# Kernel tuning notes

Hardware: AMD Instinct MI355X
Metric: run time of the kernel (lower is better)

Reference implementation:

```python
import jax, jax.numpy as jnp
import numpy as np


def setup_inputs() -> dict:
    key = jax.random.key(0)
    k1, k2 = jax.random.split(key)
    B, C, N = 8, 11, 64  # batch, fragment channels, cubic voxel grid edge
    inp = jax.random.normal(k1, (B, C, N, N, N), dtype=jnp.float32)
    tar = jax.random.normal(k2, (B, C, N, N, N), dtype=jnp.float32)
    # 20 contiguous bins spanning [-4, 4]; bin_range[k] = (lo_k, hi_k)
    edges = jnp.linspace(-4.0, 4.0, 21, dtype=jnp.float32)
    bin_range = jnp.stack([edges[:-1], edges[1:]], axis=-1)  # [20, 2]
    return {"inp": inp, "tar": tar, "bin_range": bin_range}


def _bin_data(x, bin_range):
    # x: [B, C, nx, ny, nz] -> normalized histogram [B, C, K]
    B, C = x.shape[0], x.shape[1]
    nvox = x.shape[2] * x.shape[3] * x.shape[4]
    xf = x.reshape(B, C, -1)  # [B, C, nvox]

    def count_one_bin(b):  # b: [2] = (lo, hi)
        return jnp.sum((xf >= b[0]) & (xf < b[1]), axis=-1).astype(jnp.float32)

    # sequential over K bins (small, fixed) to avoid a [K,B,C,nvox] mask blowup
    counts = jax.lax.map(count_one_bin, bin_range)  # [K, B, C]
    return jnp.transpose(counts, (1, 2, 0)) / jnp.float32(nvox)


def _smooth_l1(a, b):
    # torch.nn.SmoothL1Loss default: beta=1.0, mean reduction
    d = jnp.abs(a - b)
    return jnp.mean(jnp.where(d < 1.0, 0.5 * d * d, d - 0.5))


def reference(inp, tar, bin_range):
    loss1 = _smooth_l1(inp, tar)
    loss2 = jnp.mean(jnp.abs(_bin_data(inp, bin_range) - _bin_data(tar, bin_range)))
    return 0.5 * loss1 + 0.5 * loss2
```

## Files before the change

kernel.cpp:

```cpp
#include <hip/hip_runtime.h>

#define BC 88
#define NVOX 262144
#define KBINS 20
#define THREADS 256
#define NBLOCKS 1024
#define CPB 22
#define CPC 256
#define HSTRIDE 23
#define ROWSET (64 * HSTRIDE)

__global__ void __launch_bounds__(THREADS)
binloss_main(const float* __restrict__ inp, const float* __restrict__ tar,
             const float* __restrict__ br, int* __restrict__ slot,
             int* __restrict__ bslot, float* __restrict__ partials)
{
    __shared__ int   rows[2 * ROWSET];
    __shared__ int   qsum[2][4][KBINS];
    __shared__ float wsum[THREADS / 64];

    const int tid  = threadIdx.x;
    const int lane = tid & 63;
    for (int i = tid; i < 2 * ROWSET; i += THREADS) rows[i] = 0;

    const float e0     = br[0];
    const float eK     = br[2 * KBINS - 1];
    const float inv_w  = (float)KBINS / (eK - e0);
    const float shift1 = 1.0f - e0 * inv_w;
    const float tmax   = 21.5f;
    __syncthreads();

    const int fc  = blockIdx.x * CPB;
    const int ch0 = fc >> 8;
    const int rem = fc & (CPC - 1);
    const int n1  = (rem + CPB > CPC) ? (CPC - rem) : CPB;

    const float4* pa = (const float4*)inp + (size_t)fc * 256 + tid;
    const float4* pb = (const float4*)tar + (size_t)fc * 256 + tid;

    int* r0 = &rows[lane * HSTRIDE];
    int* r1 = r0 + ROWSET;

    float s_lin = 0.f, s_quad = 0.f;

#pragma unroll 2
    for (int k = 0; k < CPB; ++k) {
        float4 a = pa[k * 256];
        float4 b = pb[k * 256];
        int* rw = (k < n1) ? r0 : r1;
#pragma unroll
        for (int q = 0; q < 4; ++q) {
            float av = (&a.x)[q], bv = (&b.x)[q];
            float d = fabsf(av - bv);
            s_lin += fmaxf(d, 1.0f);
            float m = fminf(d, 1.0f);
            s_quad  = __builtin_fmaf(m, m, s_quad);
            int sa = (int)__builtin_amdgcn_fmed3f(__builtin_fmaf(av, inv_w, shift1), 0.0f, tmax);
            int sb = (int)__builtin_amdgcn_fmed3f(__builtin_fmaf(bv, inv_w, shift1), 0.0f, tmax);
            atomicAdd(&rw[sa], 1);
            atomicAdd(&rw[sb], -1);
        }
    }

    float sl1 = (s_lin - (float)(CPB * 4)) + 0.5f * s_quad;
#pragma unroll
    for (int off = 32; off > 0; off >>= 1) sl1 += __shfl_down(sl1, off, 64);
    if (lane == 0) wsum[tid >> 6] = sl1;
    __syncthreads();

    if (tid < 160) {
        const int set = tid / 80, r = tid % 80;
        const int qr = r / KBINS, j = r % KBINS;
        int s = 0;
#pragma unroll
        for (int rr = qr * 16; rr < qr * 16 + 16; ++rr)
            s += rows[set * ROWSET + rr * HSTRIDE + 1 + j];
        qsum[set][qr][j] = s;
    }
    if (tid == 0)
        partials[blockIdx.x] = wsum[0] + wsum[1] + wsum[2] + wsum[3];
    __syncthreads();

    if (tid < 2 * KBINS) {
        const int set = tid / KBINS, j = tid % KBINS;
        int v = qsum[set][0][j] + qsum[set][1][j] + qsum[set][2][j] + qsum[set][3][j];
        if (set == 0)          slot[blockIdx.x * KBINS + j] = v;
        else if (n1 < CPB)     bslot[(ch0 + 1) * KBINS + j] = v;
    }
    if (rem == 0 && tid < KBINS) bslot[ch0 * KBINS + tid] = 0;
}

__global__ void __launch_bounds__(256)
binloss_final(const int* __restrict__ slot, const int* __restrict__ bslot,
              const float* __restrict__ partials, float* __restrict__ out)
{
    __shared__ double r1[256];
    __shared__ double r2[256];
    const int tid = threadIdx.x;
    double s1 = 0.0, s2 = 0.0;
    for (int i = tid; i < NBLOCKS; i += 256) s1 += (double)partials[i];
    for (int i = tid; i < BC * KBINS; i += 256) {
        const int c = i / KBINS, j = i - c * KBINS;
        const int b0 = (128 * c + 10) / 11;
        const int b1 = (128 * (c + 1) + 10) / 11;
        int s = bslot[c * KBINS + j];
        for (int b = b0; b < b1; ++b) s += slot[b * KBINS + j];
        s2 += fabs((double)s);
    }
    r1[tid] = s1; r2[tid] = s2;
    __syncthreads();
    for (int off = 128; off > 0; off >>= 1) {
        if (tid < off) { r1[tid] += r1[tid + off]; r2[tid] += r2[tid + off]; }
        __syncthreads();
    }
    if (tid == 0) {
        const double ntot  = (double)BC * (double)NVOX;
        double loss1 = r1[0] / ntot;
        double loss2 = r2[0] / ((double)NVOX * (double)(BC * KBINS));
        out[0] = (float)(0.5 * loss1 + 0.5 * loss2);
    }
}

extern "C" void kernel_launch(void* const* d_in, const int* in_sizes, int n_in,
                              void* d_out, int out_size, void* d_ws, size_t ws_size,
                              hipStream_t stream) {
    const float* inp = (const float*)d_in[0];
    const float* tar = (const float*)d_in[1];
    const float* br  = (const float*)d_in[2];

    int*   slot     = (int*)d_ws;
    int*   bslot    = slot + NBLOCKS * KBINS;
    float* partials = (float*)(bslot + BC * KBINS);

    binloss_main<<<NBLOCKS, THREADS, 0, stream>>>(inp, tar, br, slot, bslot, partials);
    binloss_final<<<1, 256, 0, stream>>>(slot, bslot, partials, (float*)d_out);
}
```

Before: 51.41 us.

## Count target histogram via wave ballot-popcount and halve work per block

Target values are no longer binned with LDS atomics. Each wave instead counts, for every one of the 21 bin edges, how many values fall below that edge using ballot plus popcount, and bin counts are taken as differences of adjacent edge counts. This halves the LDS atomic traffic. In exchange it adds 21 compare/ballot/popcount steps per target element and 21 extra registers. The grid is also doubled to 2048 blocks with 11 chunks each, and the final kernel's block-to-channel mapping is updated to match.

```diff
diff --git a/kernel.cpp b/kernel.cpp
--- a/kernel.cpp
+++ b/kernel.cpp
@@ -3,9 +3,10 @@
 #define BC 88
 #define NVOX 262144
 #define KBINS 20
+#define NEDGE 21
 #define THREADS 256
-#define NBLOCKS 1024
-#define CPB 22
+#define NBLOCKS 2048
+#define CPB 11
 #define CPC 256
 #define HSTRIDE 23
 #define ROWSET (64 * HSTRIDE)
@@ -16,17 +17,20 @@
              int* __restrict__ bslot, float* __restrict__ partials)
 {
     __shared__ int   rows[2 * ROWSET];
+    __shared__ int   bcnt[2][4][NEDGE];
     __shared__ int   qsum[2][4][KBINS];
-    __shared__ float wsum[THREADS / 64];
+    __shared__ float wsum[4];
 
-    const int tid  = threadIdx.x;
-    const int lane = tid & 63;
+    const int tid = threadIdx.x, lane = tid & 63, wv = tid >> 6;
     for (int i = tid; i < 2 * ROWSET; i += THREADS) rows[i] = 0;
+    if (tid < 2 * 4 * NEDGE) ((int*)bcnt)[tid] = 0;
 
-    const float e0     = br[0];
-    const float eK     = br[2 * KBINS - 1];
-    const float inv_w  = (float)KBINS / (eK - e0);
-    const float shift1 = 1.0f - e0 * inv_w;
+    float e[NEDGE];
+#pragma unroll
+    for (int j = 0; j < KBINS; ++j) e[j] = br[2 * j];
+    e[KBINS] = br[2 * KBINS - 1];
+    const float inv_w  = (float)KBINS / (e[KBINS] - e[0]);
+    const float shift1 = 1.0f - e[0] * inv_w;
     const float tmax   = 21.5f;
     __syncthreads();
 
@@ -41,12 +45,23 @@
     int* r0 = &rows[lane * HSTRIDE];
     int* r1 = r0 + ROWSET;
 
+    int c[NEDGE];
+#pragma unroll
+    for (int j = 0; j < NEDGE; ++j) c[j] = 0;
+
     float s_lin = 0.f, s_quad = 0.f;
 
-#pragma unroll 2
+#pragma unroll
     for (int k = 0; k < CPB; ++k) {
         float4 a = pa[k * 256];
         float4 b = pb[k * 256];
+        if (k == n1) {
+            if (lane == 0)
+#pragma unroll
+                for (int j = 0; j < NEDGE; ++j) bcnt[0][wv][j] = c[j];
+#pragma unroll
+            for (int j = 0; j < NEDGE; ++j) c[j] = 0;
+        }
         int* rw = (k < n1) ? r0 : r1;
 #pragma unroll
         for (int q = 0; q < 4; ++q) {
@@ -56,16 +71,23 @@
             float m = fminf(d, 1.0f);
             s_quad  = __builtin_fmaf(m, m, s_quad);
             int sa = (int)__builtin_amdgcn_fmed3f(__builtin_fmaf(av, inv_w, shift1), 0.0f, tmax);
-            int sb = (int)__builtin_amdgcn_fmed3f(__builtin_fmaf(bv, inv_w, shift1), 0.0f, tmax);
             atomicAdd(&rw[sa], 1);
-            atomicAdd(&rw[sb], -1);
+#pragma unroll
+            for (int j = 0; j < NEDGE; ++j)
+                c[j] += (int)__popcll(__ballot(bv < e[j]));
         }
+    }
+    {
+        const int seg = (n1 < CPB) ? 1 : 0;
+        if (lane == 0)
+#pragma unroll
+            for (int j = 0; j < NEDGE; ++j) bcnt[seg][wv][j] = c[j];
     }
 
     float sl1 = (s_lin - (float)(CPB * 4)) + 0.5f * s_quad;
 #pragma unroll
     for (int off = 32; off > 0; off >>= 1) sl1 += __shfl_down(sl1, off, 64);
-    if (lane == 0) wsum[tid >> 6] = sl1;
+    if (lane == 0) wsum[wv] = sl1;
     __syncthreads();
 
     if (tid < 160) {
@@ -83,7 +105,10 @@
 
     if (tid < 2 * KBINS) {
         const int set = tid / KBINS, j = tid % KBINS;
-        int v = qsum[set][0][j] + qsum[set][1][j] + qsum[set][2][j] + qsum[set][3][j];
+        int ac  = qsum[set][0][j] + qsum[set][1][j] + qsum[set][2][j] + qsum[set][3][j];
+        int lo  = bcnt[set][0][j]     + bcnt[set][1][j]     + bcnt[set][2][j]     + bcnt[set][3][j];
+        int hi  = bcnt[set][0][j + 1] + bcnt[set][1][j + 1] + bcnt[set][2][j + 1] + bcnt[set][3][j + 1];
+        int v = ac - (hi - lo);
         if (set == 0)          slot[blockIdx.x * KBINS + j] = v;
         else if (n1 < CPB)     bslot[(ch0 + 1) * KBINS + j] = v;
     }
@@ -101,8 +126,8 @@
     for (int i = tid; i < NBLOCKS; i += 256) s1 += (double)partials[i];
     for (int i = tid; i < BC * KBINS; i += 256) {
         const int c = i / KBINS, j = i - c * KBINS;
-        const int b0 = (128 * c + 10) / 11;
-        const int b1 = (128 * (c + 1) + 10) / 11;
+        const int b0 = (256 * c + 10) / 11;
+        const int b1 = (256 * (c + 1) + 10) / 11;
         int s = bslot[c * KBINS + j];
         for (int b = b0; b < b1; ++b) s += slot[b * KBINS + j];
         s2 += fabs((double)s);
```

Measured after the change: 90.94 us. 1.77x slower.
